# Kernel tuning notes

Hardware: AMD Instinct MI355X
Metric: run time of the kernel (lower is better)

## Reference

```python
import jax, jax.numpy as jnp
import numpy as np

B, N, H = 512, 128, 256      # graphs, nodes per graph, hidden
NH, HD = 8, 32               # heads, head dim
DEG = 8
E = B * N * DEG              # 524288 edges
BN_EPS = 1e-5


def setup_inputs() -> dict:
    key = jax.random.key(0)
    ks = jax.random.split(key, 16)

    def w(k, shape):
        return jax.random.normal(k, shape, dtype=jnp.float32) * 0.02

    # intra-graph random edges: base offset per graph, local src/dst in [0, N)
    base = jnp.repeat(jnp.arange(B, dtype=jnp.int32) * N, N * DEG)
    edge_src = base + jax.random.randint(ks[1], (E,), 0, N, dtype=jnp.int32)
    edge_dst = base + jax.random.randint(ks[2], (E,), 0, N, dtype=jnp.int32)

    return {
        "h": jax.random.normal(ks[0], (B * N, H), dtype=jnp.float32),
        "edge_src": edge_src,
        "edge_dst": edge_dst,
        "gin_w1": w(ks[3], (H, H)), "gin_b1": jnp.zeros((H,), jnp.float32),
        "gin_w2": w(ks[4], (H, H)), "gin_b2": jnp.zeros((H,), jnp.float32),
        "attn_in_w": w(ks[5], (3 * H, H)), "attn_in_b": jnp.zeros((3 * H,), jnp.float32),
        "attn_out_w": w(ks[6], (H, H)), "attn_out_b": jnp.zeros((H,), jnp.float32),
        "bn_local_g": jnp.ones((H,), jnp.float32), "bn_local_b": jnp.zeros((H,), jnp.float32),
        "bn_attn_g": jnp.ones((H,), jnp.float32), "bn_attn_b": jnp.zeros((H,), jnp.float32),
        "bn_out_g": jnp.ones((H,), jnp.float32), "bn_out_b": jnp.zeros((H,), jnp.float32),
        "ffn1_w": w(ks[7], (2 * H, H)), "ffn1_b": jnp.zeros((2 * H,), jnp.float32),
        "ffn2_w": w(ks[8], (H, 2 * H)), "ffn2_b": jnp.zeros((H,), jnp.float32),
    }


def _bn(x, g, b):
    # nn.BatchNorm1d training-mode forward: batch stats over node dim, biased var
    mean = jnp.mean(x, axis=0)
    var = jnp.mean(jnp.square(x - mean), axis=0)
    return g * (x - mean) * jax.lax.rsqrt(var + BN_EPS) + b


def _mha(x, in_w, in_b, out_w, out_b):
    # x: [B, N, H]; uniform graphs -> key_padding_mask is all-valid
    qkv = x @ in_w.T + in_b                           # [B, N, 3H]
    q, k, v = jnp.split(qkv, 3, axis=-1)
    def heads(t):
        return t.reshape(B, N, NH, HD).transpose(0, 2, 1, 3)  # [B, NH, N, HD]
    q, k, v = heads(q), heads(k), heads(v)
    scores = jnp.einsum('bhqd,bhkd->bhqk', q, k) / jnp.sqrt(jnp.float32(HD))
    att = jax.nn.softmax(scores, axis=-1)
    o = jnp.einsum('bhqk,bhkd->bhqd', att, v).transpose(0, 2, 1, 3).reshape(B, N, H)
    return o @ out_w.T + out_b


def reference(h, edge_src, edge_dst,
              gin_w1, gin_b1, gin_w2, gin_b2,
              attn_in_w, attn_in_b, attn_out_w, attn_out_b,
              bn_local_g, bn_local_b, bn_attn_g, bn_attn_b, bn_out_g, bn_out_b,
              ffn1_w, ffn1_b, ffn2_w, ffn2_b):
    # --- local GIN branch: (1+eps)*h + sum_{j in N(i)} h_j, eps=0, then 2-layer MLP
    agg = jax.ops.segment_sum(h[edge_src], edge_dst, num_segments=B * N)
    z = h + agg
    h_local = jax.nn.relu(z @ gin_w1.T + gin_b1) @ gin_w2.T + gin_b2
    h_local = _bn(h + h_local, bn_local_g, bn_local_b)

    # --- global attention branch (to_dense_batch is an exact reshape here)
    h_dense = h.reshape(B, N, H)
    h_attn = _mha(h_dense, attn_in_w, attn_in_b, attn_out_w, attn_out_b).reshape(B * N, H)
    h_attn = _bn(h + h_attn, bn_attn_g, bn_attn_b)

    # --- combine + FFN + out norm
    x = h_local + h_attn
    x = x + jax.nn.relu(x @ ffn1_w.T + ffn1_b) @ ffn2_w.T + ffn2_b
    return _bn(x, bn_out_g, bn_out_b)
```

## Files before the change

### kernel.cpp

```cpp
#include <hip/hip_runtime.h>
#include <hip/hip_bf16.h>

#define B_   512
#define N_   128
#define H_   256
#define NH_  8
#define HD_  32
#define DEG_ 8
#define R_   (B_ * N_)
#define E_   (B_ * N_ * DEG_)
#define EPG_ (N_ * DEG_)

typedef unsigned short u16;
typedef unsigned int u32;

typedef __attribute__((ext_vector_type(8))) short s16x8;
typedef __attribute__((ext_vector_type(4))) float f32x4;

__device__ __forceinline__ float b2f(u16 u) {
  union { u32 i; float f; } v;
  v.i = ((u32)u) << 16;
  return v.f;
}
__device__ __forceinline__ u16 f2b(float f) {
  union { float f; u32 u; } v;
  v.f = f;
  u32 r = (v.u + 0x7fffu + ((v.u >> 16) & 1u)) >> 16;
  return (u16)r;
}
__device__ __forceinline__ void ld4b(const u16* p, float* o) {
  ushort4 v = *(const ushort4*)p;
  o[0] = b2f(v.x); o[1] = b2f(v.y); o[2] = b2f(v.z); o[3] = b2f(v.w);
}

__device__ __forceinline__ int tix(int row, int col) {
  return ((row >> 7) << 15) + (((col >> 6) & 3) << 13) + ((row & 127) << 6) +
         (((((col >> 3) & 7) ^ (row & 7))) << 3) + (col & 7);
}

__device__ __forceinline__ void glds16(const u16* g, u16* l) {
  __builtin_amdgcn_global_load_lds(
      (const __attribute__((address_space(1))) void*)g,
      (__attribute__((address_space(3))) void*)l, 16, 0, 0);
}


#define OFF_GW1 0
#define OFF_GB1 65536
#define OFF_GW2 65792
#define OFF_GB2 131328
#define OFF_AIW 131584
#define OFF_AIB 328192
#define OFF_AOW 328960
#define OFF_AOB 394496
#define OFF_F1W 394752
#define OFF_F1B 525824
#define OFF_F2W 526336
#define OFF_F2B 657408
#define W_TOTAL 657664

__global__ void zero_stats(float* __restrict__ st) {
  st[blockIdx.x * 256 + threadIdx.x] = 0.f;
}

__global__ __launch_bounds__(256) void cvt_h(const float* __restrict__ src,
                                             u16* __restrict__ dst) {
  const int e = (blockIdx.x * 256 + threadIdx.x) * 4;
  const float4 v = *(const float4*)(src + e);
  ushort4 o;
  o.x = f2b(v.x); o.y = f2b(v.y); o.z = f2b(v.z); o.w = f2b(v.w);
  *(ushort4*)(dst + tix(e >> 8, e & 255)) = o;
}

__global__ __launch_bounds__(256) void cvt_w(
    const float* s0, const float* s1, const float* s2, const float* s3,
    const float* s4, const float* s5, const float* s6, const float* s7,
    const float* s8, const float* s9, const float* s10, const float* s11,
    u16* __restrict__ dst) {
  const int sizes[12] = {65536, 256, 65536, 256, 196608, 768,
                         65536, 256, 131072, 512, 131072, 256};
  const float* srcs[12] = {s0, s1, s2, s3, s4, s5, s6, s7, s8, s9, s10, s11};
  int gid = (blockIdx.x * 256 + threadIdx.x) * 4;
  if (gid >= W_TOTAL) return;
  int seg = 0, off = gid;
  while (off >= sizes[seg]) { off -= sizes[seg]; seg++; }
  const float4 v = *(const float4*)(srcs[seg] + off);
  ushort4 o;
  o.x = f2b(v.x); o.y = f2b(v.y); o.z = f2b(v.z); o.w = f2b(v.w);
  *(ushort4*)(dst + gid) = o;
}

#define SROWS_ 32

__global__ __launch_bounds__(256) void agg_kernel(
    const u16* __restrict__ h, const int* __restrict__ esrc,
    const int* __restrict__ edst, u16* __restrict__ z) {
  __shared__ int s_src[EPG_];
  __shared__ int s_cnt[SROWS_];
  __shared__ int s_off[SROWS_ + 1];
  __shared__ int s_pos[SROWS_];
  const int g = blockIdx.x;
  const int r0 = blockIdx.y * SROWS_;
  const int t = threadIdx.x;

  if (t < SROWS_) s_cnt[t] = 0;
  __syncthreads();

  const int ebase = g * EPG_;
  int dl[4], sg[4];
#pragma unroll
  for (int i = 0; i < 4; i++) {
    const int e = ebase + t + i * 256;
    sg[i] = esrc[e];
    dl[i] = edst[e] - g * N_ - r0;
    if ((unsigned)dl[i] < SROWS_) atomicAdd(&s_cnt[dl[i]], 1);
  }
  __syncthreads();
  if (t == 0) {
    int acc = 0;
#pragma unroll
    for (int i = 0; i < SROWS_; i++) { s_off[i] = acc; acc += s_cnt[i]; }
    s_off[SROWS_] = acc;
  }
  __syncthreads();
  if (t < SROWS_) s_pos[t] = s_off[t];
  __syncthreads();
#pragma unroll
  for (int i = 0; i < 4; i++) {
    if ((unsigned)dl[i] < SROWS_) {
      const int slot = atomicAdd(&s_pos[dl[i]], 1);
      s_src[slot] = sg[i];
    }
  }
  __syncthreads();

  const int rg = t >> 5;
  const int c0 = (t & 31) * 8;
  for (int ib = 0; ib < SROWS_; ib += 8) {
    const int i = ib + rg;
    const int row = g * N_ + r0 + i;
    float acc[8];
    {
      const s16x8 v = *(const s16x8*)(h + tix(row, c0));
#pragma unroll
      for (int j = 0; j < 8; j++) acc[j] = b2f((u16)v[j]);
    }
    const int e0 = s_off[i], e1 = s_off[i + 1];
    for (int e = e0; e < e1; e++) {
      const int src = s_src[e];
      const s16x8 v = *(const s16x8*)(h + tix(src, c0));
#pragma unroll
      for (int j = 0; j < 8; j++) acc[j] += b2f((u16)v[j]);
    }
    s16x8 o;
#pragma unroll
    for (int j = 0; j < 8; j++) o[j] = (short)f2b(acc[j]);
    *(s16x8*)(z + tix(row, c0)) = o;
  }
}

template <int NC, int K, int RELU, int RES, int STATS, int ASPLIT, int CMODE>
__global__ __launch_bounds__(256) void gemm_mfma(
    const u16* A, const u16* A2,
    const u16* __restrict__ W, const u16* __restrict__ bias,
    const u16* res, u16* C0, u16* C1, u16* C2,
    float* __restrict__ gsum, float* __restrict__ gsq) {
  __shared__ u16 As[2][64 * 64] __attribute__((aligned(16)));
  __shared__ u16 Bs[2][64 * 64] __attribute__((aligned(16)));

  const int t = threadIdx.x;
  const int wave = t >> 6, lane = t & 63;
  const int wr = wave >> 1, wc = wave & 1;
  const int quad = lane >> 4, ln15 = lane & 15;
  const int row0 = blockIdx.y * 64, col0 = blockIdx.x * 64;

  f32x4 acc[2][2];
#pragma unroll
  for (int i = 0; i < 2; i++)
#pragma unroll
    for (int j = 0; j < 2; j++) acc[i][j] = (f32x4){0.f, 0.f, 0.f, 0.f};

  auto stage = [&](int b, int kt) {
    const u16* Ab;
    int ksl;
    if (ASPLIT) {
      if (kt < 256) { Ab = A; ksl = kt >> 6; } else { Ab = A2; ksl = (kt - 256) >> 6; }
    } else {
      Ab = A; ksl = kt >> 6;
    }
    const u16* abase = Ab + ((size_t)(row0 >> 7) << 15) + (ksl << 13) +
                       ((row0 & 64) << 6);
#pragma unroll
    for (int i = 0; i < 2; i++) {
      const int fid = t + i * 256;
      glds16(abase + fid * 8, &As[b][fid * 8]);
      const int row = fid >> 3;
      const int segp = (fid & 7) ^ (row & 7);
      glds16(W + (size_t)(col0 + row) * K + kt + segp * 8, &Bs[b][fid * 8]);
    }
  };

  stage(0, 0);
  for (int kt = 0; kt < K; kt += 64) {
    const int cur = (kt >> 6) & 1;
    if (kt + 64 < K) {
      stage(cur ^ 1, kt + 64);
      asm volatile("s_waitcnt vmcnt(4)" ::: "memory");
    } else {
      asm volatile("s_waitcnt vmcnt(0)" ::: "memory");
    }
    __builtin_amdgcn_s_barrier();
#pragma unroll
    for (int ks = 0; ks < 64; ks += 32) {
      s16x8 af[2], bf[2];
#pragma unroll
      for (int i = 0; i < 2; i++) {
        const int ra = wr * 32 + i * 16 + ln15;
        af[i] = *(const s16x8*)(
            &As[cur][ra * 64 + ((((ks >> 3) + quad) ^ (ra & 7)) * 8)]);
      }
#pragma unroll
      for (int j = 0; j < 2; j++) {
        const int rb = wc * 32 + j * 16 + ln15;
        bf[j] = *(const s16x8*)(
            &Bs[cur][rb * 64 + ((((ks >> 3) + quad) ^ (rb & 7)) * 8)]);
      }
#pragma unroll
      for (int i = 0; i < 2; i++)
#pragma unroll
        for (int j = 0; j < 2; j++)
          acc[i][j] = __builtin_amdgcn_mfma_f32_16x16x32_bf16(af[i], bf[j], acc[i][j], 0, 0, 0);
    }
    __builtin_amdgcn_s_barrier();
  }

  const int cbase = col0 + wc * 32;
  u16* Cb;
  int coff;
  if (CMODE) {
    const int chunk = col0 >> 8;
    Cb = (chunk == 0) ? C0 : ((chunk == 1) ? C1 : C2);
    coff = (col0 & 255) + wc * 32;
  } else {
    Cb = C0; coff = cbase;
  }

  float bs[2];
#pragma unroll
  for (int j = 0; j < 2; j++) bs[j] = b2f(bias[cbase + j * 16 + ln15]);

  float ssum[2] = {}, ssq[2] = {};
#pragma unroll
  for (int i = 0; i < 2; i++) {
    const int rbase = row0 + wr * 32 + i * 16 + quad * 4;
#pragma unroll
    for (int reg = 0; reg < 4; reg++) {
      const int row = rbase + reg;
#pragma unroll
      for (int j = 0; j < 2; j++) {
        float val = acc[i][j][reg] + bs[j];
        if (RELU) val = fmaxf(val, 0.f);
        if (RES) val += b2f(res[tix(row, cbase + j * 16 + ln15)]);
        Cb[tix(row, coff + j * 16 + ln15)] = f2b(val);
        if (STATS) { ssum[j] += val; ssq[j] += val * val; }
      }
    }
  }

  if (STATS) {
#pragma unroll
    for (int j = 0; j < 2; j++) {
      float s = ssum[j];
      s += __shfl_xor(s, 16);
      s += __shfl_xor(s, 32);
      float q = ssq[j];
      q += __shfl_xor(q, 16);
      q += __shfl_xor(q, 32);
      if (lane < 16) {
        atomicAdd(&gsum[cbase + j * 16 + lane], s);
        atomicAdd(&gsq[cbase + j * 16 + lane], q);
      }
    }
  }
}

template <int CHUNKS, int RES_LDS, int COMBINE>
__global__ __launch_bounds__(256, 2) void fused_mlp(
    const u16* A, const u16* Ara,
    const u16* __restrict__ W1, const u16* __restrict__ b1,
    const u16* __restrict__ W2, const u16* __restrict__ b2,
    const u16* resg, u16* C, const float* __restrict__ st,
    float* __restrict__ gsum, float* __restrict__ gsq) {
  __shared__ u16 xs[4 * 64 * 64] __attribute__((aligned(16)));
  __shared__ u16 tc[64 * 128] __attribute__((aligned(16)));
  __shared__ u16 Wst[2][128 * 64] __attribute__((aligned(16)));

  const int t = threadIdx.x;
  const int wave = t >> 6, lane = t & 63;
  const int wr = wave >> 1, wc = wave & 1;
  const int quad = lane >> 4, ln15 = lane & 15;
  const int row0 = blockIdx.x * 64;
  const int K2 = CHUNKS * 128;

  if (COMBINE) {
    float* cf = (float*)tc;
#pragma unroll
    for (int k = 0; k < 4; k++) cf[k * 256 + t] = st[1536 + k * 256 + t];
    __syncthreads();
    const size_t tbase = ((size_t)(row0 >> 7) << 15) + ((row0 & 64) << 6);
#pragma unroll
    for (int i = 0; i < 8; i++) {
      const int gid = t + i * 256;
      const int kstep = gid >> 9;
      const int fid = gid & 511;
      const size_t addr = tbase + kstep * 8192 + fid * 8;
      const s16x8 rl = *(const s16x8*)(A + addr);
      const s16x8 ra = *(const s16x8*)(Ara + addr);
      const int seg = (fid & 7) ^ ((fid >> 3) & 7);
      const int col = kstep * 64 + seg * 8;
      const float4 al0 = *(const float4*)(cf + col);
      const float4 al1 = *(const float4*)(cf + col + 4);
      const float4 bl0 = *(const float4*)(cf + 256 + col);
      const float4 bl1 = *(const float4*)(cf + 256 + col + 4);
      const float4 aa0 = *(const float4*)(cf + 512 + col);
      const float4 aa1 = *(const float4*)(cf + 512 + col + 4);
      const float4 ba0 = *(const float4*)(cf + 768 + col);
      const float4 ba1 = *(const float4*)(cf + 768 + col + 4);
      const float al[8] = {al0.x, al0.y, al0.z, al0.w, al1.x, al1.y, al1.z, al1.w};
      const float bl[8] = {bl0.x, bl0.y, bl0.z, bl0.w, bl1.x, bl1.y, bl1.z, bl1.w};
      const float aa[8] = {aa0.x, aa0.y, aa0.z, aa0.w, aa1.x, aa1.y, aa1.z, aa1.w};
      const float ba[8] = {ba0.x, ba0.y, ba0.z, ba0.w, ba1.x, ba1.y, ba1.z, ba1.w};
      s16x8 o;
#pragma unroll
      for (int j = 0; j < 8; j++)
        o[j] = (short)f2b(al[j] * b2f((u16)rl[j]) + bl[j] +
                          aa[j] * b2f((u16)ra[j]) + ba[j]);
      *(s16x8*)(xs + gid * 8) = o;
    }
    __syncthreads();
  } else {
    const u16* abase = A + ((size_t)(row0 >> 7) << 15) + ((row0 & 64) << 6);
#pragma unroll
    for (int i = 0; i < 8; i++) {
      const int gid = t + i * 256;
      const int kstep = gid >> 9;
      const int fid = gid & 511;
      glds16(abase + kstep * 8192 + fid * 8, xs + gid * 8);
    }
  }

  f32x4 acc2[2][8];
#pragma unroll
  for (int i = 0; i < 2; i++)
#pragma unroll
    for (int j = 0; j < 8; j++) acc2[i][j] = (f32x4){0.f, 0.f, 0.f, 0.f};

  auto tca = [&](int row, int col) {
    const int s0 = col >> 3;
    return row * 128 + (((s0 & 8) | ((s0 ^ row) & 7)) << 3) + (col & 7);
  };

  for (int c = 0; c < CHUNKS; c++) {
    f32x4 acc1[2][4];
#pragma unroll
    for (int i = 0; i < 2; i++)
#pragma unroll
      for (int j = 0; j < 4; j++) acc1[i][j] = (f32x4){0.f, 0.f, 0.f, 0.f};

    auto stage1 = [&](int b, int kt) {
#pragma unroll
      for (int i = 0; i < 4; i++) {
        const int fid = t + i * 256;
        const int row = fid >> 3;
        const int segp = (fid & 7) ^ (row & 7);
        glds16(W1 + (size_t)(c * 128 + row) * 256 + kt + segp * 8,
               &Wst[b][fid * 8]);
      }
    };

    stage1(0, 0);
    for (int kt = 0; kt < 256; kt += 64) {
      const int cur = (kt >> 6) & 1;
      if (kt + 64 < 256) {
        stage1(cur ^ 1, kt + 64);
        asm volatile("s_waitcnt vmcnt(4)" ::: "memory");
      } else {
        asm volatile("s_waitcnt vmcnt(0)" ::: "memory");
      }
      __builtin_amdgcn_s_barrier();
#pragma unroll
      for (int ks = 0; ks < 64; ks += 32) {
        s16x8 af[2], bf[4];
#pragma unroll
        for (int i = 0; i < 2; i++) {
          const int ra = wr * 32 + i * 16 + ln15;
          af[i] = *(const s16x8*)(
              &xs[(kt >> 6) * 4096 + ra * 64 +
                  ((((ks >> 3) + quad) ^ (ra & 7)) * 8)]);
        }
#pragma unroll
        for (int j = 0; j < 4; j++) {
          const int rb = wc * 64 + j * 16 + ln15;
          bf[j] = *(const s16x8*)(
              &Wst[cur][rb * 64 + ((((ks >> 3) + quad) ^ (rb & 7)) * 8)]);
        }
#pragma unroll
        for (int i = 0; i < 2; i++)
#pragma unroll
          for (int j = 0; j < 4; j++)
            acc1[i][j] = __builtin_amdgcn_mfma_f32_16x16x32_bf16(af[i], bf[j], acc1[i][j], 0, 0, 0);
      }
      __builtin_amdgcn_s_barrier();
    }

    {
      float b1s[4];
#pragma unroll
      for (int j = 0; j < 4; j++)
        b1s[j] = b2f(b1[c * 128 + wc * 64 + j * 16 + ln15]);
#pragma unroll
      for (int i = 0; i < 2; i++)
#pragma unroll
        for (int reg = 0; reg < 4; reg++) {
          const int rowl = wr * 32 + i * 16 + quad * 4 + reg;
#pragma unroll
          for (int j = 0; j < 4; j++) {
            const int coll = wc * 64 + j * 16 + ln15;
            tc[tca(rowl, coll)] = f2b(fmaxf(acc1[i][j][reg] + b1s[j], 0.f));
          }
        }
    }
    __syncthreads();

    for (int ks2 = 0; ks2 < 2; ks2++) {
#pragma unroll
      for (int i = 0; i < 8; i++) {
        const int fid = t + i * 256;
        const int row = fid >> 3;
        const int segp = (fid & 7) ^ (row & 7);
        glds16(W2 + (size_t)row * K2 + c * 128 + ks2 * 64 + segp * 8,
               &Wst[0][fid * 8]);
      }
      asm volatile("s_waitcnt vmcnt(0)" ::: "memory");
      __builtin_amdgcn_s_barrier();
#pragma unroll
      for (int ksl = 0; ksl < 64; ksl += 32) {
        s16x8 af[2], bf[8];
#pragma unroll
        for (int i = 0; i < 2; i++) {
          const int ra = wr * 32 + i * 16 + ln15;
          af[i] = *(const s16x8*)(&tc[tca(ra, ks2 * 64 + ksl + quad * 8)]);
        }
#pragma unroll
        for (int j = 0; j < 8; j++) {
          const int rb = wc * 128 + j * 16 + ln15;
          bf[j] = *(const s16x8*)(
              &Wst[0][rb * 64 + ((((ksl >> 3) + quad) ^ (rb & 7)) * 8)]);
        }
#pragma unroll
        for (int i = 0; i < 2; i++)
#pragma unroll
          for (int j = 0; j < 8; j++)
            acc2[i][j] = __builtin_amdgcn_mfma_f32_16x16x32_bf16(af[i], bf[j], acc2[i][j], 0, 0, 0);
      }
      __builtin_amdgcn_s_barrier();
    }
  }

  float bs2[8];
#pragma unroll
  for (int j = 0; j < 8; j++)
    bs2[j] = b2f(b2[wc * 128 + j * 16 + ln15]);

  float ssum[8] = {}, ssq[8] = {};
#pragma unroll
  for (int i = 0; i < 2; i++) {
#pragma unroll
    for (int reg = 0; reg < 4; reg++) {
      const int rowl = wr * 32 + i * 16 + quad * 4 + reg;
      const int row = row0 + rowl;
#pragma unroll
      for (int j = 0; j < 8; j++) {
        const int col = wc * 128 + j * 16 + ln15;
        float val = acc2[i][j][reg] + bs2[j];
        if (RES_LDS) {
          val += b2f(xs[(col >> 6) * 4096 + rowl * 64 +
                        ((((col >> 3) & 7) ^ (rowl & 7)) << 3) + (col & 7)]);
        } else {
          val += b2f(resg[tix(row, col)]);
        }
        C[tix(row, col)] = f2b(val);
        ssum[j] += val; ssq[j] += val * val;
      }
    }
  }

#pragma unroll
  for (int j = 0; j < 8; j++) {
    float s = ssum[j];
    s += __shfl_xor(s, 16);
    s += __shfl_xor(s, 32);
    float q = ssq[j];
    q += __shfl_xor(q, 16);
    q += __shfl_xor(q, 32);
    if (lane < 16) {
      atomicAdd(&gsum[wc * 128 + j * 16 + lane], s);
      atomicAdd(&gsq[wc * 128 + j * 16 + lane], q);
    }
  }
}

__global__ __launch_bounds__(256) void attn_mfma(
    const u16* q, const u16* __restrict__ k,
    const u16* __restrict__ v, u16* o) {
  __shared__ u16 lds[21760] __attribute__((aligned(16)));
  u16* Vt = lds;
  u16* Qs = lds + 4352;
  u16* Ks = lds + 4352 + 5120;
  u16* P  = lds + 4352;

  const int g = blockIdx.x >> 3;
  const int hd = blockIdx.x & 7;
  const int t = threadIdx.x;
  const int wave = t >> 6, lane = t & 63;
  const int quad = lane >> 4, ln15 = lane & 15;
  const int strip = wave * 32;
  const float scale = 0.1767766952966369f;

#pragma unroll
  for (int i = 0; i < 4; i++) {
    const int fid = t + i * 256;
    const int row = fid >> 3;
    const int seg = fid & 7;
    const int gidx = tix(g * N_ + row, hd * HD_ + seg * 4);
    const ushort4 qv = *(const ushort4*)(q + gidx);
    const ushort4 kv = *(const ushort4*)(k + gidx);
    const ushort4 vv = *(const ushort4*)(v + gidx);
    ushort4 qs;
    qs.x = f2b(b2f(qv.x) * scale); qs.y = f2b(b2f(qv.y) * scale);
    qs.z = f2b(b2f(qv.z) * scale); qs.w = f2b(b2f(qv.w) * scale);
    *(ushort4*)(Qs + row * 40 + seg * 4) = qs;
    *(ushort4*)(Ks + row * 40 + seg * 4) = kv;
    Vt[(seg * 4 + 0) * 136 + row] = vv.x;
    Vt[(seg * 4 + 1) * 136 + row] = vv.y;
    Vt[(seg * 4 + 2) * 136 + row] = vv.z;
    Vt[(seg * 4 + 3) * 136 + row] = vv.w;
  }
  __syncthreads();

  s16x8 af[2], bf[8];
#pragma unroll
  for (int mi = 0; mi < 2; mi++)
    af[mi] = *(const s16x8*)(Qs + (strip + mi * 16 + ln15) * 40 + quad * 8);
#pragma unroll
  for (int nj = 0; nj < 8; nj++)
    bf[nj] = *(const s16x8*)(Ks + (nj * 16 + ln15) * 40 + quad * 8);

  f32x4 acc[2][8];
#pragma unroll
  for (int mi = 0; mi < 2; mi++)
#pragma unroll
    for (int nj = 0; nj < 8; nj++)
      acc[mi][nj] = __builtin_amdgcn_mfma_f32_16x16x32_bf16(
          af[mi], bf[nj], (f32x4){0.f, 0.f, 0.f, 0.f}, 0, 0, 0);

  __syncthreads();

#pragma unroll
  for (int mi = 0; mi < 2; mi++) {
#pragma unroll
    for (int reg = 0; reg < 4; reg++) {
      float mx = acc[mi][0][reg];
#pragma unroll
      for (int j = 1; j < 8; j++) mx = fmaxf(mx, acc[mi][j][reg]);
      mx = fmaxf(mx, __shfl_xor(mx, 1));
      mx = fmaxf(mx, __shfl_xor(mx, 2));
      mx = fmaxf(mx, __shfl_xor(mx, 4));
      mx = fmaxf(mx, __shfl_xor(mx, 8));
      float e[8], s = 0.f;
#pragma unroll
      for (int j = 0; j < 8; j++) { e[j] = __expf(acc[mi][j][reg] - mx); s += e[j]; }
      s += __shfl_xor(s, 1);
      s += __shfl_xor(s, 2);
      s += __shfl_xor(s, 4);
      s += __shfl_xor(s, 8);
      const float inv = 1.f / s;
      const int prow = strip + mi * 16 + quad * 4 + reg;
#pragma unroll
      for (int j = 0; j < 8; j++)
        P[prow * 136 + j * 16 + ln15] = f2b(e[j] * inv);
    }
  }
  __syncthreads();

  f32x4 acc2[2][2];
#pragma unroll
  for (int mi = 0; mi < 2; mi++)
#pragma unroll
    for (int nj = 0; nj < 2; nj++) acc2[mi][nj] = (f32x4){0.f, 0.f, 0.f, 0.f};
#pragma unroll
  for (int kt = 0; kt < 4; kt++) {
    s16x8 paf[2], vbf[2];
#pragma unroll
    for (int mi = 0; mi < 2; mi++)
      paf[mi] = *(const s16x8*)(P + (strip + mi * 16 + ln15) * 136 + kt * 32 + quad * 8);
#pragma unroll
    for (int nj = 0; nj < 2; nj++)
      vbf[nj] = *(const s16x8*)(Vt + (nj * 16 + ln15) * 136 + kt * 32 + quad * 8);
#pragma unroll
    for (int mi = 0; mi < 2; mi++)
#pragma unroll
      for (int nj = 0; nj < 2; nj++)
        acc2[mi][nj] = __builtin_amdgcn_mfma_f32_16x16x32_bf16(
            paf[mi], vbf[nj], acc2[mi][nj], 0, 0, 0);
  }

#pragma unroll
  for (int mi = 0; mi < 2; mi++)
#pragma unroll
    for (int nj = 0; nj < 2; nj++)
#pragma unroll
      for (int reg = 0; reg < 4; reg++) {
        const int row = strip + mi * 16 + quad * 4 + reg;
        o[tix(g * N_ + row, hd * HD_ + nj * 16 + ln15)] =
            f2b(acc2[mi][nj][reg]);
      }
}

__global__ void bn_finalize(const float* __restrict__ sum,
                            const float* __restrict__ sq,
                            const float* __restrict__ g,
                            const float* __restrict__ bb,
                            float* __restrict__ a, float* __restrict__ b) {
  const int c = threadIdx.x;
  const float mean = sum[c] * (1.f / R_);
  const float var = fmaxf(sq[c] * (1.f / R_) - mean * mean, 0.f);
  const float ai = g[c] * rsqrtf(var + 1e-5f);
  a[c] = ai;
  b[c] = bb[c] - mean * ai;
}

__global__ __launch_bounds__(256) void final_kernel(
    const u16* __restrict__ y, const float* __restrict__ st,
    float* __restrict__ out) {
  const int e = (blockIdx.x * 256 + threadIdx.x) * 4;
  const int col = e & 255;
  float y4[4];
  ld4b(y + tix(e >> 8, col), y4);
  const float* ao = st + 2560;
  const float* bo = st + 2816;
  float4 o;
  o.x = ao[col + 0] * y4[0] + bo[col + 0];
  o.y = ao[col + 1] * y4[1] + bo[col + 1];
  o.z = ao[col + 2] * y4[2] + bo[col + 2];
  o.w = ao[col + 3] * y4[3] + bo[col + 3];
  *(float4*)(out + e) = o;
}

extern "C" void kernel_launch(void* const* d_in, const int* in_sizes, int n_in,
                              void* d_out, int out_size, void* d_ws, size_t ws_size,
                              hipStream_t stream) {
  const float* h = (const float*)d_in[0];
  const int* esrc = (const int*)d_in[1];
  const int* edst = (const int*)d_in[2];
  const float* bn_local_g = (const float*)d_in[11];
  const float* bn_local_b = (const float*)d_in[12];
  const float* bn_attn_g = (const float*)d_in[13];
  const float* bn_attn_b = (const float*)d_in[14];
  const float* bn_out_g = (const float*)d_in[15];
  const float* bn_out_b = (const float*)d_in[16];

  const size_t RH = (size_t)R_ * H_;
  float* stats = (float*)d_ws;
  u16* WB = (u16*)((char*)d_ws + 65536);
  u16* Hb = (u16*)((char*)d_ws + 65536 + 2097152);
  u16* S1 = Hb + RH;
  u16* S2 = S1 + RH;
  u16* OD = (u16*)d_out;
  float* outf = (float*)d_out;

  zero_stats<<<12, 256, 0, stream>>>(stats);
  cvt_h<<<(int)(RH / 4 / 256), 256, 0, stream>>>(h, Hb);
  cvt_w<<<(W_TOTAL / 4 + 255) / 256, 256, 0, stream>>>(
      (const float*)d_in[3], (const float*)d_in[4], (const float*)d_in[5],
      (const float*)d_in[6], (const float*)d_in[7], (const float*)d_in[8],
      (const float*)d_in[9], (const float*)d_in[10], (const float*)d_in[17],
      (const float*)d_in[18], (const float*)d_in[19], (const float*)d_in[20], WB);

  gemm_mfma<768, 256, 0, 0, 0, 0, 1><<<dim3(12, 1024), 256, 0, stream>>>(
      Hb, nullptr, WB + OFF_AIW, WB + OFF_AIB, nullptr, S1, S2, OD,
      nullptr, nullptr);
  attn_mfma<<<B_ * NH_, 256, 0, stream>>>(S1, S2, OD, S1);
  gemm_mfma<256, 256, 0, 1, 1, 0, 0><<<dim3(4, 1024), 256, 0, stream>>>(
      S1, nullptr, WB + OFF_AOW, WB + OFF_AOB, Hb, S2, nullptr, nullptr,
      stats + 512, stats + 768);
  agg_kernel<<<dim3(B_, 4), 256, 0, stream>>>(Hb, esrc, edst, OD);
  fused_mlp<2, 0, 0><<<1024, 256, 0, stream>>>(
      OD, nullptr, WB + OFF_GW1, WB + OFF_GB1, WB + OFF_GW2, WB + OFF_GB2,
      Hb, OD, nullptr, stats + 0, stats + 256);

  bn_finalize<<<1, 256, 0, stream>>>(stats + 0, stats + 256, bn_local_g,
                                     bn_local_b, stats + 1536, stats + 1792);
  bn_finalize<<<1, 256, 0, stream>>>(stats + 512, stats + 768, bn_attn_g,
                                     bn_attn_b, stats + 2048, stats + 2304);

  fused_mlp<4, 1, 1><<<1024, 256, 0, stream>>>(
      OD, S2, WB + OFF_F1W, WB + OFF_F1B, WB + OFF_F2W, WB + OFF_F2B,
      nullptr, S1, stats, stats + 1024, stats + 1280);

  bn_finalize<<<1, 256, 0, stream>>>(stats + 1024, stats + 1280, bn_out_g,
                                     bn_out_b, stats + 2560, stats + 2816);
  final_kernel<<<(int)(RH / 4 / 256), 256, 0, stream>>>(S1, stats, outf);
}
```

Baseline: 545.7 us.

## Pipeline W1/W2 weight staging across chunks with double-buffered 32-wide slices

Restructures weight staging in fused_mlp so the W2 slices and the next chunk's first W1 tile are prefetched into double-buffered LDS while the current MFMA work runs. Previously each W2 half was loaded with a full vmcnt(0) wait before compute. W2 is now staged in 32-column slices with a new XOR swizzle, so the LDS footprint stays the same. The cost is more barriers and a more intricate waitcnt scheme, which risks ordering mistakes.

```diff
diff --git a/kernel.cpp b/kernel.cpp
--- a/kernel.cpp
+++ b/kernel.cpp
@@ -293,7 +293,7 @@
     float* __restrict__ gsum, float* __restrict__ gsq) {
   __shared__ u16 xs[4 * 64 * 64] __attribute__((aligned(16)));
   __shared__ u16 tc[64 * 128] __attribute__((aligned(16)));
-  __shared__ u16 Wst[2][128 * 64] __attribute__((aligned(16)));
+  __shared__ u16 Wst[2][64 * 128] __attribute__((aligned(16)));
 
   const int t = threadIdx.x;
   const int wave = t >> 6, lane = t & 63;
@@ -301,6 +301,30 @@
   const int quad = lane >> 4, ln15 = lane & 15;
   const int row0 = blockIdx.x * 64;
   const int K2 = CHUNKS * 128;
+
+  auto stage1 = [&](int b, int ch, int kt) {
+#pragma unroll
+    for (int i = 0; i < 4; i++) {
+      const int fid = t + i * 256;
+      const int row = fid >> 3;
+      const int segp = (fid & 7) ^ (row & 7);
+      glds16(W1 + (size_t)(ch * 128 + row) * 256 + kt + segp * 8,
+             &Wst[b][fid * 8]);
+    }
+  };
+  auto stageW2s = [&](int b, int ch, int ks) {
+#pragma unroll
+    for (int i = 0; i < 4; i++) {
+      const int fid = t + i * 256;
+      const int row = fid >> 2;
+      const int sg = fid & 3;
+      const int segp = sg ^ ((row >> 2) & 3);
+      glds16(W2 + (size_t)row * K2 + ch * 128 + ks * 32 + segp * 8,
+             &Wst[b][fid * 8]);
+    }
+  };
+
+  stage1(0, 0, 0);
 
   if (COMBINE) {
     float* cf = (float*)tc;
@@ -367,26 +391,14 @@
 #pragma unroll
       for (int j = 0; j < 4; j++) acc1[i][j] = (f32x4){0.f, 0.f, 0.f, 0.f};
 
-    auto stage1 = [&](int b, int kt) {
-#pragma unroll
-      for (int i = 0; i < 4; i++) {
-        const int fid = t + i * 256;
-        const int row = fid >> 3;
-        const int segp = (fid & 7) ^ (row & 7);
-        glds16(W1 + (size_t)(c * 128 + row) * 256 + kt + segp * 8,
-               &Wst[b][fid * 8]);
-      }
-    };
-
-    stage1(0, 0);
     for (int kt = 0; kt < 256; kt += 64) {
       const int cur = (kt >> 6) & 1;
-      if (kt + 64 < 256) {
-        stage1(cur ^ 1, kt + 64);
-        asm volatile("s_waitcnt vmcnt(4)" ::: "memory");
+      if (kt < 192) {
+        stage1(cur ^ 1, c, kt + 64);
       } else {
-        asm volatile("s_waitcnt vmcnt(0)" ::: "memory");
-      }
+        stageW2s(0, c, 0);
+      }
+      asm volatile("s_waitcnt vmcnt(4)" ::: "memory");
       __builtin_amdgcn_s_barrier();
 #pragma unroll
       for (int ks = 0; ks < 64; ks += 32) {
@@ -413,6 +425,8 @@
       __builtin_amdgcn_s_barrier();
     }
 
+    stageW2s(1, c, 1);
+
     {
       float b1s[4];
 #pragma unroll
@@ -430,40 +444,47 @@
           }
         }
     }
-    __syncthreads();
-
-    for (int ks2 = 0; ks2 < 2; ks2++) {
-#pragma unroll
-      for (int i = 0; i < 8; i++) {
-        const int fid = t + i * 256;
-        const int row = fid >> 3;
-        const int segp = (fid & 7) ^ (row & 7);
-        glds16(W2 + (size_t)row * K2 + c * 128 + ks2 * 64 + segp * 8,
-               &Wst[0][fid * 8]);
-      }
-      asm volatile("s_waitcnt vmcnt(0)" ::: "memory");
+    asm volatile("s_waitcnt lgkmcnt(0)" ::: "memory");
+    asm volatile("s_waitcnt vmcnt(4)" ::: "memory");
+    __builtin_amdgcn_s_barrier();
+
+#pragma unroll
+    for (int s = 0; s < 4; s++) {
+      s16x8 af[2], bf[8];
+#pragma unroll
+      for (int i = 0; i < 2; i++) {
+        const int ra = wr * 32 + i * 16 + ln15;
+        af[i] = *(const s16x8*)(&tc[tca(ra, s * 32 + quad * 8)]);
+      }
+#pragma unroll
+      for (int j = 0; j < 8; j++) {
+        const int rb = wc * 128 + j * 16 + ln15;
+        bf[j] = *(const s16x8*)(
+            &Wst[s & 1][rb * 32 + ((quad ^ ((rb >> 2) & 3)) * 8)]);
+      }
+#pragma unroll
+      for (int i = 0; i < 2; i++)
+#pragma unroll
+        for (int j = 0; j < 8; j++)
+          acc2[i][j] = __builtin_amdgcn_mfma_f32_16x16x32_bf16(af[i], bf[j], acc2[i][j], 0, 0, 0);
       __builtin_amdgcn_s_barrier();
-#pragma unroll
-      for (int ksl = 0; ksl < 64; ksl += 32) {
-        s16x8 af[2], bf[8];
-#pragma unroll
-        for (int i = 0; i < 2; i++) {
-          const int ra = wr * 32 + i * 16 + ln15;
-          af[i] = *(const s16x8*)(&tc[tca(ra, ks2 * 64 + ksl + quad * 8)]);
+      if (s == 0) {
+        stageW2s(0, c, 2);
+        asm volatile("s_waitcnt vmcnt(4)" ::: "memory");
+        __builtin_amdgcn_s_barrier();
+      } else if (s == 1) {
+        stageW2s(1, c, 3);
+        asm volatile("s_waitcnt vmcnt(4)" ::: "memory");
+        __builtin_amdgcn_s_barrier();
+      } else if (s == 2) {
+        if (c + 1 < CHUNKS) {
+          stage1(0, c + 1, 0);
+          asm volatile("s_waitcnt vmcnt(4)" ::: "memory");
+        } else {
+          asm volatile("s_waitcnt vmcnt(0)" ::: "memory");
         }
-#pragma unroll
-        for (int j = 0; j < 8; j++) {
-          const int rb = wc * 128 + j * 16 + ln15;
-          bf[j] = *(const s16x8*)(
-              &Wst[0][rb * 64 + ((((ksl >> 3) + quad) ^ (rb & 7)) * 8)]);
-        }
-#pragma unroll
-        for (int i = 0; i < 2; i++)
-#pragma unroll
-          for (int j = 0; j < 8; j++)
-            acc2[i][j] = __builtin_amdgcn_mfma_f32_16x16x32_bf16(af[i], bf[j], acc2[i][j], 0, 0, 0);
-      }
-      __builtin_amdgcn_s_barrier();
+        __builtin_amdgcn_s_barrier();
+      }
     }
   }
 
```

New measurement: 546.9 us. About the same (+0.2%).
